# Optimization experiments

Hardware: AMD Instinct MI355X
Metric: run time of the kernel (lower is better)

Reference implementation:

```python
import jax, jax.numpy as jnp
import numpy as np
import math

D = 1024      # model dim
H = 16        # heads
DK = D // H   # 64
FF = 4096     # ff_dim
B, T = 2, 2048


def _norm(x, alpha, bias, eps=1e-6):
    # torch: (x - mean) / (x.std(unbiased) + eps) * alpha + bias
    mu = jnp.mean(x, axis=-1, keepdims=True)
    sd = jnp.std(x, axis=-1, keepdims=True, ddof=1)  # unbiased, like torch
    return alpha * ((x - mu) / (sd + eps)) + bias


def setup_inputs() -> dict:
    key = jax.random.key(0)
    ks = jax.random.split(key, 20)
    w = lambda k, shp: (jax.random.normal(k, shp, jnp.float32) * 0.02)
    inp = {
        "x": jax.random.normal(ks[0], (B, T, D), jnp.float32),
        "x_mask": jnp.ones((B, T), jnp.int32),  # unused by the module's forward
        "Wq": w(ks[1], (D, D)), "bq": jnp.zeros((D,), jnp.float32),
        "Wk": w(ks[2], (D, D)), "bk": jnp.zeros((D,), jnp.float32),
        "Wv": w(ks[3], (D, D)), "bv": jnp.zeros((D,), jnp.float32),
        "Wo": w(ks[4], (D, D)), "bo": jnp.zeros((D,), jnp.float32),
        "W1": w(ks[5], (D, FF)), "b1": jnp.zeros((FF,), jnp.float32),
        "W2": w(ks[6], (FF, D)), "b2": jnp.zeros((D,), jnp.float32),
        "alpha1": jnp.ones((D,), jnp.float32), "beta1": jnp.zeros((D,), jnp.float32),
        "alpha2": jnp.ones((D,), jnp.float32), "beta2": jnp.zeros((D,), jnp.float32),
    }
    return inp


def reference(x, x_mask, Wq, bq, Wk, bk, Wv, bv, Wo, bo,
              W1, b1, W2, b2, alpha1, beta1, alpha2, beta2):
    b, t, d = x.shape
    # projections -> [B, H, T, DK]
    q = (x @ Wq + bq).reshape(b, t, H, DK).swapaxes(1, 2)
    k = (x @ Wk + bk).reshape(b, t, H, DK).swapaxes(1, 2)
    v = (x @ Wv + bv).reshape(b, t, H, DK).swapaxes(1, 2)
    # eager attention: QK^T / sqrt(dk), clamp_min(-6000), softmax (no mask used)
    score = jnp.einsum('bhqd,bhkd->bhqk', q, k) / math.sqrt(DK)
    score = jnp.maximum(score, -6000.0)
    score = jax.nn.softmax(score, axis=-1)  # dropout=identity at inference
    val = jnp.einsum('bhqk,bhkd->bhqd', score, v)
    val = val.swapaxes(1, 2).reshape(b, t, d)
    attn_out = val @ Wo + bo
    # residual + norm1 (dropout identity)
    xn = _norm(x + attn_out, alpha1, beta1)
    # FFN: relu(linear1) -> linear2
    ff = jnp.maximum(xn @ W1 + b1, 0.0) @ W2 + b2
    out = _norm(xn + ff, alpha2, beta2)
    return out, score
```

## Files before the change

### kernel.cpp

```cpp
#include <hip/hip_runtime.h>
#include <stdint.h>

#define T_SEQ   2048
#define D_MODEL 1024
#define N_HEADS 16
#define D_HEAD  64
#define FF_DIM  4096
#define BATCH   2
#define BT      (BATCH * T_SEQ)

#define QSCALE 0.18033688011112042f

typedef unsigned short u16;
typedef __attribute__((ext_vector_type(8))) short bf16x8;
typedef __attribute__((ext_vector_type(4))) float f32x4;
typedef __attribute__((ext_vector_type(16))) float f32x16;

__device__ __forceinline__ u16 f2bf(float f) {
  union { float f; unsigned u; } x; x.f = f;
  unsigned r = x.u + 0x7fffu + ((x.u >> 16) & 1u);
  return (u16)(r >> 16);
}

__device__ __forceinline__ void gload16(const void* g, void* l) {
  __builtin_amdgcn_global_load_lds(
      (const __attribute__((address_space(1))) void*)g,
      (__attribute__((address_space(3))) void*)l, 16, 0, 0);
}

struct PrepArgs {
  const float* x; u16* xb;
  const float *Wq, *Wk, *Wv, *Wo, *W1, *W2;
  u16 *WqT, *WkT, *WvT, *WoT, *W1T, *W2T;
};

__global__ __launch_bounds__(256)
void prep_kernel(PrepArgs pa) {
  const int bid = blockIdx.x;
  const int tid = threadIdx.x;
  if (bid < 4096) {
    int i = (bid * 256 + tid) * 4;
    float4 v = *(const float4*)(pa.x + i);
    ushort4 o; o.x = f2bf(v.x); o.y = f2bf(v.y); o.z = f2bf(v.z); o.w = f2bf(v.w);
    *(ushort4*)(pa.xb + i) = o;
    return;
  }
  int t = bid - 4096;
  const float* W; u16* Wt; int K, N, rel;
  if (t < 1024)      { W = pa.Wq; Wt = pa.WqT; K = 1024; N = 1024; rel = t; }
  else if (t < 2048) { W = pa.Wk; Wt = pa.WkT; K = 1024; N = 1024; rel = t - 1024; }
  else if (t < 3072) { W = pa.Wv; Wt = pa.WvT; K = 1024; N = 1024; rel = t - 2048; }
  else if (t < 4096) { W = pa.Wo; Wt = pa.WoT; K = 1024; N = 1024; rel = t - 3072; }
  else if (t < 8192) { W = pa.W1; Wt = pa.W1T; K = 1024; N = 4096; rel = t - 4096; }
  else               { W = pa.W2; Wt = pa.W2T; K = 4096; N = 1024; rel = t - 8192; }
  const int ntn = N >> 5;
  const int n0 = (rel % ntn) * 32, k0 = (rel / ntn) * 32;
  const int tx = tid & 31, ty = tid >> 5;
  __shared__ float tile[32][33];
#pragma unroll
  for (int r = 0; r < 4; ++r)
    tile[ty + r * 8][tx] = W[(size_t)(k0 + ty + r * 8) * N + n0 + tx];
  __syncthreads();
#pragma unroll
  for (int r = 0; r < 4; ++r)
    Wt[(size_t)(n0 + ty + r * 8) * K + k0 + tx] = f2bf(tile[tx][ty + r * 8]);
}

struct GemmArgs {
  const u16* A;
  const u16* B0; const u16* B1; const u16* B2;
  const float* bias0; const float* bias1; const float* bias2;
  void* out0; void* out1; void* out2;
  int M, N, K;
};

template <int EPI>
__global__ __launch_bounds__(256, 3)
void gemm_bt(GemmArgs ga) {
  const int tid = threadIdx.x;
  const int gx = gridDim.x, gy = gridDim.y;
  const int nwg = gx * gy * gridDim.z;
  const int orig = blockIdx.x + gx * (blockIdx.y + gy * blockIdx.z);
  const int swz = (orig & 7) * (nwg >> 3) + (orig >> 3);
  const int bx = swz % gx, by = (swz / gx) % gy, bz = swz / (gx * gy);
  const int m0 = by * 128;
  const int n0 = bx * 128;
  const int lane = tid & 63, w = tid >> 6;
  const int wr = w >> 1, wc = w & 1;
  const int l15 = lane & 15, g = lane >> 4;

  const u16* Bt; const float* bias; void* outp;
  int z = 0;
  if (EPI == 0) {
    z = bz;
    Bt   = (z == 0) ? ga.B0   : (z == 1) ? ga.B1   : ga.B2;
    bias = (z == 0) ? ga.bias0 : (z == 1) ? ga.bias1 : ga.bias2;
    outp = (z == 0) ? ga.out0 : (z == 1) ? ga.out1 : ga.out2;
  } else if (EPI == 3) {
    z = bz; Bt = ga.B0; bias = nullptr; outp = ga.out0;
  } else { Bt = ga.B0; bias = ga.bias0; outp = ga.out0; }

  __shared__ char lsA[128 * 128];
  __shared__ char lsB[128 * 128];

  f32x4 acc[4][4] = {};
  const int K = ga.K;
  const int kbase = (EPI == 3) ? z * (K >> 1) : 0;
  const int nk = (EPI == 3) ? (K >> 7) : (K >> 6);

  auto stage = [&](int kt) {
    const int k0 = kbase + kt * 64;
#pragma unroll
    for (int i = 0; i < 4; ++i) {
      int o = i * 4096 + tid * 16;
      int row = o >> 7, cb = o & 127;
      int lcb = cb ^ ((row & 7) << 4);
      gload16((const char*)ga.A + ((size_t)(m0 + row) * K + k0) * 2 + lcb, lsA + o);
    }
#pragma unroll
    for (int i = 0; i < 4; ++i) {
      int o = i * 4096 + tid * 16;
      int row = o >> 7, cb = o & 127;
      int lcb = cb ^ ((row & 7) << 4);
      gload16((const char*)Bt + ((size_t)(n0 + row) * K + k0) * 2 + lcb, lsB + o);
    }
  };

  stage(0);
  for (int kt = 0; kt < nk; ++kt) {
    __syncthreads();
#pragma unroll
    for (int kk = 0; kk < 2; ++kk) {
      bf16x8 a[4], b[4];
#pragma unroll
      for (int mi = 0; mi < 4; ++mi) {
        int row = wr * 64 + mi * 16 + l15;
        a[mi] = *(const bf16x8*)(lsA + row * 128 + ((kk * 64 + g * 16) ^ ((row & 7) << 4)));
      }
#pragma unroll
      for (int ni = 0; ni < 4; ++ni) {
        int row = wc * 64 + ni * 16 + l15;
        b[ni] = *(const bf16x8*)(lsB + row * 128 + ((kk * 64 + g * 16) ^ ((row & 7) << 4)));
      }
#pragma unroll
      for (int mi = 0; mi < 4; ++mi)
#pragma unroll
        for (int ni = 0; ni < 4; ++ni)
          acc[mi][ni] = __builtin_amdgcn_mfma_f32_16x16x32_bf16(a[mi], b[ni], acc[mi][ni], 0, 0, 0);
    }
    __syncthreads();
    if (kt + 1 < nk) stage(kt + 1);
  }

  const int N = ga.N;
#pragma unroll
  for (int mi = 0; mi < 4; ++mi) {
#pragma unroll
    for (int ni = 0; ni < 4; ++ni) {
      const int c = n0 + wc * 64 + ni * 16 + l15;
      const float bv = (EPI == 3) ? 0.0f : bias[c];
#pragma unroll
      for (int j = 0; j < 4; ++j) {
        const int r = m0 + wr * 64 + mi * 16 + g * 4 + j;
        float v = acc[mi][ni][j] + bv;
        if constexpr (EPI == 0) {
          if (z == 0) v *= QSCALE;
          const int bb = r >> 11, t = r & 2047, hh = c >> 6, dk = c & 63;
          u16* o = (u16*)outp;
          size_t idx = (z < 2)
              ? ((size_t)((bb * N_HEADS + hh) * T_SEQ + t)) * D_HEAD + dk
              : ((size_t)((bb * N_HEADS + hh) * D_HEAD + dk)) * T_SEQ + t;
          o[idx] = f2bf(v);
        } else if constexpr (EPI == 3) {
          ((float*)outp)[(size_t)z * ga.M * N + (size_t)r * N + c] = v;
        } else {
          ((u16*)outp)[(size_t)r * N + c] = f2bf(fmaxf(v, 0.0f));
        }
      }
    }
  }
}

__global__ __launch_bounds__(128, 2)
void attn_kernel(const u16* __restrict__ q, const u16* __restrict__ k,
                 const u16* __restrict__ vT, float* __restrict__ score,
                 u16* __restrict__ val) {
  const int tid = threadIdx.x;
  const int lane = tid & 63, w = tid >> 6;
  const int l31 = lane & 31, hi = lane >> 5;
  const int nwg = gridDim.x;
  const int orig = blockIdx.x;
  const int swz = (orig & 7) * (nwg >> 3) + (orig >> 3);
  const int bh = swz >> 5;
  const int Q0 = (swz & 31) * 64;
  const size_t hoff = (size_t)bh * T_SEQ * D_HEAD;
  const u16* qb = q + hoff;
  const u16* kb = k + hoff;
  const u16* vb = vT + hoff;
  float* sb = score + ((size_t)bh * T_SEQ + Q0) * T_SEQ;

  __shared__ char lsK[128 * 128];
  __shared__ char lsV[64 * 256];
  __shared__ char lsP[2][32 * 128];

  auto stageK = [&](int jt) {
    const int J0 = jt * 128;
#pragma unroll
    for (int i = 0; i < 8; ++i) {
      int o = i * 2048 + tid * 16;
      int row = o >> 7, cb = o & 127;
      int lcb = cb ^ ((row & 7) << 4);
      gload16((const char*)kb + ((size_t)(J0 + row) * D_HEAD) * 2 + lcb, lsK + o);
    }
  };
  auto stageV = [&](int jt) {
    const int J0 = jt * 128;
#pragma unroll
    for (int i = 0; i < 8; ++i) {
      int o = i * 2048 + tid * 16;
      int row = o >> 8, cb = o & 255;
      int lcb = cb ^ ((row & 15) << 4);
      gload16((const char*)vb + ((size_t)row * T_SEQ + J0) * 2 + lcb, lsV + o);
    }
  };

  bf16x8 qf[4];
  {
    int row = Q0 + w * 32 + l31;
#pragma unroll
    for (int ks = 0; ks < 4; ++ks)
      qf[ks] = *(const bf16x8*)(qb + (size_t)row * D_HEAD + ks * 16 + hi * 8);
  }

  float lsum[16];
#pragma unroll
  for (int r = 0; r < 16; ++r) lsum[r] = 0.f;

  for (int jt = 0; jt < 16; ++jt) {
    __syncthreads();
    stageK(jt);
    __syncthreads();
#pragma unroll
    for (int st = 0; st < 4; ++st) {
      f32x16 c = {};
      __builtin_amdgcn_s_setprio(1);
#pragma unroll
      for (int ks = 0; ks < 4; ++ks) {
        int row = st * 32 + l31;
        bf16x8 b = *(const bf16x8*)(lsK + row * 128 + ((ks * 32 + hi * 16) ^ ((row & 7) << 4)));
        c = __builtin_amdgcn_mfma_f32_32x32x16_bf16(qf[ks], b, c, 0, 0, 0);
      }
      __builtin_amdgcn_s_setprio(0);
#pragma unroll
      for (int r = 0; r < 16; ++r)
        lsum[r] += __builtin_amdgcn_exp2f(c[r]);
    }
  }
  float inv[16];
#pragma unroll
  for (int r = 0; r < 16; ++r) {
    float v = lsum[r];
    v += __shfl_xor(v, 1);
    v += __shfl_xor(v, 2);
    v += __shfl_xor(v, 4);
    v += __shfl_xor(v, 8);
    v += __shfl_xor(v, 16);
    inv[r] = 1.0f / v;
  }

  f32x16 vacc[2] = {};
  char* myP = lsP[w];

  for (int jt = 0; jt < 16; ++jt) {
    const int J0 = jt * 128;
    __syncthreads();
    stageK(jt);
    stageV(jt);
    __syncthreads();
#pragma unroll
    for (int h = 0; h < 2; ++h) {
#pragma unroll
      for (int st = 0; st < 2; ++st) {
        f32x16 c = {};
        __builtin_amdgcn_s_setprio(1);
#pragma unroll
        for (int ks = 0; ks < 4; ++ks) {
          int row = h * 64 + st * 32 + l31;
          bf16x8 b = *(const bf16x8*)(lsK + row * 128 + ((ks * 32 + hi * 16) ^ ((row & 7) << 4)));
          c = __builtin_amdgcn_mfma_f32_32x32x16_bf16(qf[ks], b, c, 0, 0, 0);
        }
        __builtin_amdgcn_s_setprio(0);
#pragma unroll
        for (int r = 0; r < 16; ++r) {
          int rr = (r & 3) + 8 * (r >> 2) + 4 * hi;
          float p = __builtin_amdgcn_exp2f(c[r]) * inv[r];
          __builtin_nontemporal_store(
              p, &sb[(size_t)(w * 32 + rr) * T_SEQ + J0 + h * 64 + st * 32 + l31]);
          *(u16*)(myP + rr * 128 + (((st * 32 + l31) * 2) ^ ((rr & 7) << 4))) = f2bf(p);
        }
      }
#pragma unroll
      for (int ks = 0; ks < 4; ++ks) {
        bf16x8 pa = *(const bf16x8*)(myP + l31 * 128 + ((ks * 32 + hi * 16) ^ ((l31 & 7) << 4)));
        __builtin_amdgcn_s_setprio(1);
#pragma unroll
        for (int ct = 0; ct < 2; ++ct) {
          int vrow = ct * 32 + l31;
          bf16x8 vf = *(const bf16x8*)(lsV + vrow * 256 +
                                       ((h * 128 + ks * 32 + hi * 16) ^ ((vrow & 15) << 4)));
          vacc[ct] = __builtin_amdgcn_mfma_f32_32x32x16_bf16(pa, vf, vacc[ct], 0, 0, 0);
        }
        __builtin_amdgcn_s_setprio(0);
      }
    }
  }

  const int bb = bh >> 4, hh = bh & 15;
#pragma unroll
  for (int ct = 0; ct < 2; ++ct)
#pragma unroll
    for (int r = 0; r < 16; ++r) {
      int rr = (r & 3) + 8 * (r >> 2) + 4 * hi;
      int qrow = Q0 + w * 32 + rr;
      val[((size_t)(bb * T_SEQ + qrow)) * D_MODEL + hh * D_HEAD + ct * 32 + l31] =
          f2bf(vacc[ct][r]);
    }
}

template <bool WRITE_BF16>
__global__ __launch_bounds__(256)
void norm_kernel(const float* __restrict__ p0, const float* __restrict__ p1,
                 const float* __restrict__ bias, const float* __restrict__ resid,
                 const float* __restrict__ alpha, const float* __restrict__ beta,
                 float* __restrict__ outf, u16* __restrict__ outb) {
  const int row = blockIdx.x;
  const int tid = threadIdx.x;
  const size_t base = (size_t)row * D_MODEL + tid * 4;
  float4 v0 = *(const float4*)(p0 + base);
  float4 v1 = *(const float4*)(p1 + base);
  float4 bi = *(const float4*)(bias + tid * 4);
  float4 rs = *(const float4*)(resid + base);
  float4 v;
  v.x = v0.x + v1.x + bi.x + rs.x;
  v.y = v0.y + v1.y + bi.y + rs.y;
  v.z = v0.z + v1.z + bi.z + rs.z;
  v.w = v0.w + v1.w + bi.w + rs.w;
  float s = v.x + v.y + v.z + v.w;
  float ss = v.x * v.x + v.y * v.y + v.z * v.z + v.w * v.w;
#pragma unroll
  for (int m = 1; m < 64; m <<= 1) {
    s += __shfl_xor(s, m);
    ss += __shfl_xor(ss, m);
  }
  __shared__ float red[8];
  int w = tid >> 6, lane = tid & 63;
  if (lane == 0) { red[w] = s; red[4 + w] = ss; }
  __syncthreads();
  s = red[0] + red[1] + red[2] + red[3];
  ss = red[4] + red[5] + red[6] + red[7];
  float mu = s * (1.0f / 1024.0f);
  float var = fmaxf(ss - s * mu, 0.0f) * (1.0f / 1023.0f);
  float inv = 1.0f / (sqrtf(var) + 1e-6f);
  float4 a = *(const float4*)(alpha + tid * 4);
  float4 be = *(const float4*)(beta + tid * 4);
  float4 o;
  o.x = (v.x - mu) * inv * a.x + be.x;
  o.y = (v.y - mu) * inv * a.y + be.y;
  o.z = (v.z - mu) * inv * a.z + be.z;
  o.w = (v.w - mu) * inv * a.w + be.w;
  *(float4*)(outf + base) = o;
  if (WRITE_BF16) {
    ushort4 ob; ob.x = f2bf(o.x); ob.y = f2bf(o.y); ob.z = f2bf(o.z); ob.w = f2bf(o.w);
    *(ushort4*)(outb + base) = ob;
  }
}

extern "C" void kernel_launch(void* const* d_in, const int* in_sizes, int n_in,
                              void* d_out, int out_size, void* d_ws, size_t ws_size,
                              hipStream_t stream) {
  const float* x   = (const float*)d_in[0];
  const float* Wq  = (const float*)d_in[2];
  const float* bq  = (const float*)d_in[3];
  const float* Wk  = (const float*)d_in[4];
  const float* bk  = (const float*)d_in[5];
  const float* Wv  = (const float*)d_in[6];
  const float* bv  = (const float*)d_in[7];
  const float* Wo  = (const float*)d_in[8];
  const float* bo  = (const float*)d_in[9];
  const float* W1  = (const float*)d_in[10];
  const float* b1  = (const float*)d_in[11];
  const float* W2  = (const float*)d_in[12];
  const float* b2  = (const float*)d_in[13];
  const float* a1  = (const float*)d_in[14];
  const float* be1 = (const float*)d_in[15];
  const float* a2  = (const float*)d_in[16];
  const float* be2 = (const float*)d_in[17];

  float* out   = (float*)d_out;
  float* score = out + (size_t)BT * D_MODEL;

  char* ws = (char*)d_ws;
  const size_t MB = (size_t)1 << 20;
  u16*   xb   = (u16*)(ws + 0 * MB);
  u16*   WqT  = (u16*)(ws + 8 * MB);
  u16*   WkT  = (u16*)(ws + 10 * MB);
  u16*   WvT  = (u16*)(ws + 12 * MB);
  u16*   WoT  = (u16*)(ws + 14 * MB);
  u16*   W1T  = (u16*)(ws + 16 * MB);
  u16*   W2T  = (u16*)(ws + 24 * MB);
  u16*   qw   = (u16*)(ws + 32 * MB);
  u16*   kw   = (u16*)(ws + 40 * MB);
  u16*   vTw  = (u16*)(ws + 48 * MB);
  u16*   valw = (u16*)(ws + 56 * MB);
  float* p0   = (float*)(ws + 64 * MB);
  float* p1   = (float*)(ws + 80 * MB);
  float* xn   = (float*)(ws + 0 * MB);
  u16*   xnb  = (u16*)(ws + 96 * MB);
  u16*   hw   = (u16*)(ws + 32 * MB);

  {
    PrepArgs pa{ x, xb, Wq, Wk, Wv, Wo, W1, W2, WqT, WkT, WvT, WoT, W1T, W2T };
    prep_kernel<<<16384, 256, 0, stream>>>(pa);
  }

  {
    GemmArgs ga{};
    ga.A = xb;
    ga.B0 = WqT; ga.B1 = WkT; ga.B2 = WvT;
    ga.bias0 = bq; ga.bias1 = bk; ga.bias2 = bv;
    ga.out0 = qw; ga.out1 = kw; ga.out2 = vTw;
    ga.M = BT; ga.N = D_MODEL; ga.K = D_MODEL;
    gemm_bt<0><<<dim3(8, 32, 3), 256, 0, stream>>>(ga);
  }

  attn_kernel<<<1024, 128, 0, stream>>>(qw, kw, vTw, score, valw);

  {
    GemmArgs ga{};
    ga.A = valw; ga.B0 = WoT; ga.out0 = p0;
    ga.M = BT; ga.N = D_MODEL; ga.K = D_MODEL;
    gemm_bt<3><<<dim3(8, 32, 2), 256, 0, stream>>>(ga);
  }

  norm_kernel<true><<<BT, 256, 0, stream>>>(p0, p0 + (size_t)BT * D_MODEL, bo, x,
                                            a1, be1, xn, xnb);

  {
    GemmArgs ga{};
    ga.A = xnb; ga.B0 = W1T; ga.bias0 = b1; ga.out0 = hw;
    ga.M = BT; ga.N = FF_DIM; ga.K = D_MODEL;
    gemm_bt<2><<<dim3(32, 32, 1), 256, 0, stream>>>(ga);
  }

  {
    GemmArgs ga{};
    ga.A = hw; ga.B0 = W2T; ga.out0 = p0;
    ga.M = BT; ga.N = D_MODEL; ga.K = FF_DIM;
    gemm_bt<3><<<dim3(8, 32, 2), 256, 0, stream>>>(ga);
  }

  norm_kernel<false><<<BT, 256, 0, stream>>>(p0, p0 + (size_t)BT * D_MODEL, b2, xn,
                                             a2, be2, out, nullptr);
}
```

Before: 343.8 us.

## Split attention into fused flash PV pass and separate score-writing kernel

The attention kernel now computes the row sums and the PV product in a single pass over K/V, normalising the output at the end and saving the denominators to a workspace. A separate score kernel with 256 threads per block recomputes QK^T and writes the normalised probability matrix using those denominators. The norm kernels are also changed so the first norm writes only bf16 xn, and the second norm reads that bf16 tensor as its residual, removing one fp32 round trip. The cost is an extra QK^T pass and a second launch, and the residual now carries bf16 precision loss.

```diff
diff --git a/kernel.cpp b/kernel.cpp
--- a/kernel.cpp
+++ b/kernel.cpp
@@ -20,6 +20,11 @@
   union { float f; unsigned u; } x; x.f = f;
   unsigned r = x.u + 0x7fffu + ((x.u >> 16) & 1u);
   return (u16)(r >> 16);
+}
+
+__device__ __forceinline__ float bf2f(u16 b) {
+  union { unsigned u; float f; } x; x.u = ((unsigned)b) << 16;
+  return x.f;
 }
 
 __device__ __forceinline__ void gload16(const void* g, void* l) {
@@ -182,9 +187,9 @@
 }
 
 __global__ __launch_bounds__(128, 2)
-void attn_kernel(const u16* __restrict__ q, const u16* __restrict__ k,
-                 const u16* __restrict__ vT, float* __restrict__ score,
-                 u16* __restrict__ val) {
+void attn_flash(const u16* __restrict__ q, const u16* __restrict__ k,
+                const u16* __restrict__ vT, float* __restrict__ den,
+                u16* __restrict__ val) {
   const int tid = threadIdx.x;
   const int lane = tid & 63, w = tid >> 6;
   const int l31 = lane & 31, hi = lane >> 5;
@@ -197,7 +202,6 @@
   const u16* qb = q + hoff;
   const u16* kb = k + hoff;
   const u16* vb = vT + hoff;
-  float* sb = score + ((size_t)bh * T_SEQ + Q0) * T_SEQ;
 
   __shared__ char lsK[128 * 128];
   __shared__ char lsV[64 * 256];
@@ -235,27 +239,51 @@
   float lsum[16];
 #pragma unroll
   for (int r = 0; r < 16; ++r) lsum[r] = 0.f;
+  f32x16 vacc[2] = {};
+  char* myP = lsP[w];
 
   for (int jt = 0; jt < 16; ++jt) {
     __syncthreads();
     stageK(jt);
+    stageV(jt);
     __syncthreads();
 #pragma unroll
-    for (int st = 0; st < 4; ++st) {
-      f32x16 c = {};
-      __builtin_amdgcn_s_setprio(1);
+    for (int h = 0; h < 2; ++h) {
+#pragma unroll
+      for (int st = 0; st < 2; ++st) {
+        f32x16 c = {};
+        __builtin_amdgcn_s_setprio(1);
+#pragma unroll
+        for (int ks = 0; ks < 4; ++ks) {
+          int row = h * 64 + st * 32 + l31;
+          bf16x8 b = *(const bf16x8*)(lsK + row * 128 + ((ks * 32 + hi * 16) ^ ((row & 7) << 4)));
+          c = __builtin_amdgcn_mfma_f32_32x32x16_bf16(qf[ks], b, c, 0, 0, 0);
+        }
+        __builtin_amdgcn_s_setprio(0);
+#pragma unroll
+        for (int r = 0; r < 16; ++r) {
+          int rr = (r & 3) + 8 * (r >> 2) + 4 * hi;
+          float p = __builtin_amdgcn_exp2f(c[r]);
+          lsum[r] += p;
+          *(u16*)(myP + rr * 128 + (((st * 32 + l31) * 2) ^ ((rr & 7) << 4))) = f2bf(p);
+        }
+      }
 #pragma unroll
       for (int ks = 0; ks < 4; ++ks) {
-        int row = st * 32 + l31;
-        bf16x8 b = *(const bf16x8*)(lsK + row * 128 + ((ks * 32 + hi * 16) ^ ((row & 7) << 4)));
-        c = __builtin_amdgcn_mfma_f32_32x32x16_bf16(qf[ks], b, c, 0, 0, 0);
-      }
-      __builtin_amdgcn_s_setprio(0);
-#pragma unroll
-      for (int r = 0; r < 16; ++r)
-        lsum[r] += __builtin_amdgcn_exp2f(c[r]);
-    }
-  }
+        bf16x8 pa = *(const bf16x8*)(myP + l31 * 128 + ((ks * 32 + hi * 16) ^ ((l31 & 7) << 4)));
+        __builtin_amdgcn_s_setprio(1);
+#pragma unroll
+        for (int ct = 0; ct < 2; ++ct) {
+          int vrow = ct * 32 + l31;
+          bf16x8 vf = *(const bf16x8*)(lsV + vrow * 256 +
+                                       ((h * 128 + ks * 32 + hi * 16) ^ ((vrow & 15) << 4)));
+          vacc[ct] = __builtin_amdgcn_mfma_f32_32x32x16_bf16(pa, vf, vacc[ct], 0, 0, 0);
+        }
+        __builtin_amdgcn_s_setprio(0);
+      }
+    }
+  }
+
   float inv[16];
 #pragma unroll
   for (int r = 0; r < 16; ++r) {
@@ -265,54 +293,9 @@
     v += __shfl_xor(v, 4);
     v += __shfl_xor(v, 8);
     v += __shfl_xor(v, 16);
+    int rr = (r & 3) + 8 * (r >> 2) + 4 * hi;
+    if (l31 == 0) den[(size_t)bh * T_SEQ + Q0 + w * 32 + rr] = v;
     inv[r] = 1.0f / v;
-  }
-
-  f32x16 vacc[2] = {};
-  char* myP = lsP[w];
-
-  for (int jt = 0; jt < 16; ++jt) {
-    const int J0 = jt * 128;
-    __syncthreads();
-    stageK(jt);
-    stageV(jt);
-    __syncthreads();
-#pragma unroll
-    for (int h = 0; h < 2; ++h) {
-#pragma unroll
-      for (int st = 0; st < 2; ++st) {
-        f32x16 c = {};
-        __builtin_amdgcn_s_setprio(1);
-#pragma unroll
-        for (int ks = 0; ks < 4; ++ks) {
-          int row = h * 64 + st * 32 + l31;
-          bf16x8 b = *(const bf16x8*)(lsK + row * 128 + ((ks * 32 + hi * 16) ^ ((row & 7) << 4)));
-          c = __builtin_amdgcn_mfma_f32_32x32x16_bf16(qf[ks], b, c, 0, 0, 0);
-        }
-        __builtin_amdgcn_s_setprio(0);
-#pragma unroll
-        for (int r = 0; r < 16; ++r) {
-          int rr = (r & 3) + 8 * (r >> 2) + 4 * hi;
-          float p = __builtin_amdgcn_exp2f(c[r]) * inv[r];
-          __builtin_nontemporal_store(
-              p, &sb[(size_t)(w * 32 + rr) * T_SEQ + J0 + h * 64 + st * 32 + l31]);
-          *(u16*)(myP + rr * 128 + (((st * 32 + l31) * 2) ^ ((rr & 7) << 4))) = f2bf(p);
-        }
-      }
-#pragma unroll
-      for (int ks = 0; ks < 4; ++ks) {
-        bf16x8 pa = *(const bf16x8*)(myP + l31 * 128 + ((ks * 32 + hi * 16) ^ ((l31 & 7) << 4)));
-        __builtin_amdgcn_s_setprio(1);
-#pragma unroll
-        for (int ct = 0; ct < 2; ++ct) {
-          int vrow = ct * 32 + l31;
-          bf16x8 vf = *(const bf16x8*)(lsV + vrow * 256 +
-                                       ((h * 128 + ks * 32 + hi * 16) ^ ((vrow & 15) << 4)));
-          vacc[ct] = __builtin_amdgcn_mfma_f32_32x32x16_bf16(pa, vf, vacc[ct], 0, 0, 0);
-        }
-        __builtin_amdgcn_s_setprio(0);
-      }
-    }
   }
 
   const int bb = bh >> 4, hh = bh & 15;
@@ -323,14 +306,81 @@
       int rr = (r & 3) + 8 * (r >> 2) + 4 * hi;
       int qrow = Q0 + w * 32 + rr;
       val[((size_t)(bb * T_SEQ + qrow)) * D_MODEL + hh * D_HEAD + ct * 32 + l31] =
-          f2bf(vacc[ct][r]);
-    }
-}
-
-template <bool WRITE_BF16>
+          f2bf(vacc[ct][r] * inv[r]);
+    }
+}
+
+__global__ __launch_bounds__(256, 4)
+void score_kernel(const u16* __restrict__ q, const u16* __restrict__ k,
+                  const float* __restrict__ den, float* __restrict__ score) {
+  const int tid = threadIdx.x;
+  const int lane = tid & 63, w = tid >> 6;
+  const int l31 = lane & 31, hi = lane >> 5;
+  const int nwg = gridDim.x;
+  const int orig = blockIdx.x;
+  const int swz = (orig & 7) * (nwg >> 3) + (orig >> 3);
+  const int bh = swz >> 4;
+  const int Qb = (swz & 15) * 128;
+  const size_t hoff = (size_t)bh * T_SEQ * D_HEAD;
+  const u16* qb = q + hoff;
+  const u16* kb = k + hoff;
+  float* sb = score + ((size_t)bh * T_SEQ + Qb) * T_SEQ;
+
+  __shared__ char lsK[128 * 128];
+
+  bf16x8 qf[4];
+  {
+    int row = Qb + w * 32 + l31;
+#pragma unroll
+    for (int ks = 0; ks < 4; ++ks)
+      qf[ks] = *(const bf16x8*)(qb + (size_t)row * D_HEAD + ks * 16 + hi * 8);
+  }
+
+  float inv[16];
+#pragma unroll
+  for (int r = 0; r < 16; ++r) {
+    int rr = (r & 3) + 8 * (r >> 2) + 4 * hi;
+    inv[r] = 1.0f / den[(size_t)bh * T_SEQ + Qb + w * 32 + rr];
+  }
+
+  for (int jt = 0; jt < 16; ++jt) {
+    const int J0 = jt * 128;
+    __syncthreads();
+#pragma unroll
+    for (int i = 0; i < 4; ++i) {
+      int o = i * 4096 + tid * 16;
+      int row = o >> 7, cb = o & 127;
+      int lcb = cb ^ ((row & 7) << 4);
+      gload16((const char*)kb + ((size_t)(J0 + row) * D_HEAD) * 2 + lcb, lsK + o);
+    }
+    __syncthreads();
+#pragma unroll
+    for (int st = 0; st < 4; ++st) {
+      f32x16 c = {};
+      __builtin_amdgcn_s_setprio(1);
+#pragma unroll
+      for (int ks = 0; ks < 4; ++ks) {
+        int row = st * 32 + l31;
+        bf16x8 b = *(const bf16x8*)(lsK + row * 128 + ((ks * 32 + hi * 16) ^ ((row & 7) << 4)));
+        c = __builtin_amdgcn_mfma_f32_32x32x16_bf16(qf[ks], b, c, 0, 0, 0);
+      }
+      __builtin_amdgcn_s_setprio(0);
+#pragma unroll
+      for (int r = 0; r < 16; ++r) {
+        int rr = (r & 3) + 8 * (r >> 2) + 4 * hi;
+        float p = __builtin_amdgcn_exp2f(c[r]) * inv[r];
+        __builtin_nontemporal_store(
+            p, &sb[(size_t)(w * 32 + rr) * T_SEQ + J0 + st * 32 + l31]);
+      }
+    }
+  }
+}
+
+template <bool OUT_F32, bool OUT_BF16, bool RESID_BF16>
 __global__ __launch_bounds__(256)
 void norm_kernel(const float* __restrict__ p0, const float* __restrict__ p1,
-                 const float* __restrict__ bias, const float* __restrict__ resid,
+                 const float* __restrict__ bias, const float* __restrict__ residf,
+                 const u16* __restrict__ residb,
                  const float* __restrict__ alpha, const float* __restrict__ beta,
                  float* __restrict__ outf, u16* __restrict__ outb) {
   const int row = blockIdx.x;
@@ -339,7 +389,13 @@
   float4 v0 = *(const float4*)(p0 + base);
   float4 v1 = *(const float4*)(p1 + base);
   float4 bi = *(const float4*)(bias + tid * 4);
-  float4 rs = *(const float4*)(resid + base);
+  float4 rs;
+  if (RESID_BF16) {
+    ushort4 rb = *(const ushort4*)(residb + base);
+    rs.x = bf2f(rb.x); rs.y = bf2f(rb.y); rs.z = bf2f(rb.z); rs.w = bf2f(rb.w);
+  } else {
+    rs = *(const float4*)(residf + base);
+  }
   float4 v;
   v.x = v0.x + v1.x + bi.x + rs.x;
   v.y = v0.y + v1.y + bi.y + rs.y;
@@ -368,8 +424,8 @@
   o.y = (v.y - mu) * inv * a.y + be.y;
   o.z = (v.z - mu) * inv * a.z + be.z;
   o.w = (v.w - mu) * inv * a.w + be.w;
-  *(float4*)(outf + base) = o;
-  if (WRITE_BF16) {
+  if (OUT_F32) *(float4*)(outf + base) = o;
+  if (OUT_BF16) {
     ushort4 ob; ob.x = f2bf(o.x); ob.y = f2bf(o.y); ob.z = f2bf(o.z); ob.w = f2bf(o.w);
     *(ushort4*)(outb + base) = ob;
   }
@@ -402,7 +458,9 @@
   char* ws = (char*)d_ws;
   const size_t MB = (size_t)1 << 20;
   u16*   xb   = (u16*)(ws + 0 * MB);
+  u16*   xnb  = (u16*)(ws + 0 * MB);
   u16*   WqT  = (u16*)(ws + 8 * MB);
+  float* denw = (float*)(ws + 8 * MB);
   u16*   WkT  = (u16*)(ws + 10 * MB);
   u16*   WvT  = (u16*)(ws + 12 * MB);
   u16*   WoT  = (u16*)(ws + 14 * MB);
@@ -412,11 +470,9 @@
   u16*   kw   = (u16*)(ws + 40 * MB);
   u16*   vTw  = (u16*)(ws + 48 * MB);
   u16*   valw = (u16*)(ws + 56 * MB);
+  u16*   hw   = (u16*)(ws + 32 * MB);
   float* p0   = (float*)(ws + 64 * MB);
   float* p1   = (float*)(ws + 80 * MB);
-  float* xn   = (float*)(ws + 0 * MB);
-  u16*   xnb  = (u16*)(ws + 96 * MB);
-  u16*   hw   = (u16*)(ws + 32 * MB);
 
   {
     PrepArgs pa{ x, xb, Wq, Wk, Wv, Wo, W1, W2, WqT, WkT, WvT, WoT, W1T, W2T };
@@ -433,7 +489,9 @@
     gemm_bt<0><<<dim3(8, 32, 3), 256, 0, stream>>>(ga);
   }
 
-  attn_kernel<<<1024, 128, 0, stream>>>(qw, kw, vTw, score, valw);
+  attn_flash<<<1024, 128, 0, stream>>>(qw, kw, vTw, denw, valw);
+
+  score_kernel<<<512, 256, 0, stream>>>(qw, kw, denw, score);
 
   {
     GemmArgs ga{};
@@ -442,8 +500,8 @@
     gemm_bt<3><<<dim3(8, 32, 2), 256, 0, stream>>>(ga);
   }
 
-  norm_kernel<true><<<BT, 256, 0, stream>>>(p0, p0 + (size_t)BT * D_MODEL, bo, x,
-                                            a1, be1, xn, xnb);
+  norm_kernel<false, true, false><<<BT, 256, 0, stream>>>(
+      p0, p1, bo, x, nullptr, a1, be1, nullptr, xnb);
 
   {
     GemmArgs ga{};
@@ -459,6 +517,6 @@
     gemm_bt<3><<<dim3(8, 32, 2), 256, 0, stream>>>(ga);
   }
 
-  norm_kernel<false><<<BT, 256, 0, stream>>>(p0, p0 + (size_t)BT * D_MODEL, b2, xn,
-                                             a2, be2, out, nullptr);
-}
+  norm_kernel<true, false, true><<<BT, 256, 0, stream>>>(
+      p0, p1, b2, nullptr, xnb, a2, be2, out, nullptr);
+}
```

Result: slower. 450.2 us (+31.0%).
